# Performance work log

Measured on AMD Instinct MI355X. Metric: run time of the kernel, lower is better.

## Reference

```python
import jax, jax.numpy as jnp
import numpy as np

N, CH, K, B = 30000, 96, 81, 8
HIDDEN = max(CH // 4, 8)
EPS = 1e-5


def setup_inputs() -> dict:
    key = jax.random.key(0)
    ks = jax.random.split(key, 12)
    feats = jax.random.normal(ks[0], (N, CH), dtype=jnp.float32)
    nbr_idx = jax.random.randint(ks[1], (N, K), 0, N).astype(jnp.int32)
    batch_ids = jnp.sort(jax.random.randint(ks[2], (N,), 0, B)).astype(jnp.int32)
    s = 1.0 / np.sqrt(CH * 1.0)
    W1 = jax.random.normal(ks[3], (K, CH, CH), dtype=jnp.float32) * s
    W2 = jax.random.normal(ks[4], (K, CH, CH), dtype=jnp.float32) * s
    g1 = jnp.ones((CH,), jnp.float32); b1 = jnp.zeros((CH,), jnp.float32)
    g2 = jnp.ones((CH,), jnp.float32); b2 = jnp.zeros((CH,), jnp.float32)
    fc1_w = jax.random.normal(ks[5], (CH, HIDDEN), dtype=jnp.float32) * s
    fc1_b = jnp.zeros((HIDDEN,), jnp.float32)
    fc2_w = jax.random.normal(ks[6], (HIDDEN, CH), dtype=jnp.float32) * (1.0 / np.sqrt(HIDDEN * 1.0))
    fc2_b = jnp.zeros((CH,), jnp.float32)
    return {"feats": feats, "W1": W1, "g1": g1, "b1": b1, "W2": W2,
            "g2": g2, "b2": b2, "fc1_w": fc1_w, "fc1_b": fc1_b,
            "fc2_w": fc2_w, "fc2_b": fc2_b, "nbr_idx": nbr_idx,
            "batch_ids": batch_ids}


def _sparse_conv(x, W, nbr):
    # gather-matmul-scatter form of MinkowskiConvolution (kernel map shared):
    # g: [N, K, ch] gathered neighbor features; contract each offset's [ch,ch] weight.
    g = x[nbr]
    return jnp.einsum('nkc,kcd->nd', g, W)


def _bn(x, gamma, beta):
    mu = jnp.mean(x, axis=0)
    var = jnp.var(x, axis=0)
    return gamma * (x - mu) * jax.lax.rsqrt(var + EPS) + beta


def _se(x, batch_ids, fc1_w, fc1_b, fc2_w, fc2_b):
    # MinkowskiGlobalAvgPooling: per-sample mean over points
    sums = jax.ops.segment_sum(x, batch_ids, num_segments=B)
    cnts = jax.ops.segment_sum(jnp.ones((x.shape[0], 1), x.dtype), batch_ids, num_segments=B)
    pooled = sums / jnp.maximum(cnts, 1.0)  # [B, ch]
    w = jax.nn.relu(pooled @ fc1_w + fc1_b)
    w = jax.nn.sigmoid(w @ fc2_w + fc2_b)   # [B, ch]
    return x * w[batch_ids]                  # broadcast multiplication


def reference(feats, W1, g1, b1, W2, g2, b2, fc1_w, fc1_b, fc2_w, fc2_b,
              nbr_idx, batch_ids):
    out = jax.nn.relu(_bn(_sparse_conv(feats, W1, nbr_idx), g1, b1))
    out = _bn(_sparse_conv(out, W2, nbr_idx), g2, b2)
    out = _se(out, batch_ids, fc1_w, fc1_b, fc2_w, fc2_b)
    return jax.nn.relu(out + feats)
```

## Files before the change

### kernel.cpp

```cpp
#include <hip/hip_runtime.h>
#include <hip/hip_bf16.h>

#define NPTS 30000
#define CH 96
#define KOFF 81
#define NB 8
#define HID 24
#define EPSV 1e-5f
#define NTILE 469
#define KSPLIT 3
#define KPER 27

typedef __attribute__((ext_vector_type(8))) short bf16x8;
typedef __attribute__((ext_vector_type(4))) float f32x4;

__device__ __forceinline__ ushort f2bf(float f) {
    union { float f; unsigned int u; } x; x.f = f;
    unsigned int u = x.u;
    unsigned int r = (u + 0x7fffu + ((u >> 16) & 1u)) >> 16;
    return (ushort)r;
}

__device__ __forceinline__ void gll16(const void* g, void* l) {
    __builtin_amdgcn_global_load_lds(
        (const __attribute__((address_space(1))) unsigned int*)g,
        (__attribute__((address_space(3))) unsigned int*)l, 16, 0, 0);
}


__global__ void k_cvt_feats(const float* __restrict__ in, ushort* __restrict__ out, int n4) {
    int t = blockIdx.x * 256 + threadIdx.x;
    if (t >= n4) return;
    float4 v = reinterpret_cast<const float4*>(in)[t];
    ushort4 o;
    o.x = f2bf(v.x); o.y = f2bf(v.y); o.z = f2bf(v.z); o.w = f2bf(v.w);
    reinterpret_cast<ushort4*>(out)[t] = o;
}

__global__ void k_cvt_w(const float* __restrict__ W1, const float* __restrict__ W2,
                        ushort* __restrict__ wt1, ushort* __restrict__ wt2) {
    __shared__ float lds[9216];
    int b = blockIdx.x;
    int k = (b < 81) ? b : b - 81;
    const float* src = ((b < 81) ? W1 : W2) + k * 9216;
    ushort* dst = ((b < 81) ? wt1 : wt2) + k * 9216;
    for (int j = threadIdx.x; j < 9216; j += 256) lds[j] = src[j];
    __syncthreads();
    for (int o = threadIdx.x; o < 9216; o += 256) {
        int q = o / 768, rem = o - q * 768, d = rem >> 3, j = rem & 7;
        dst[o] = f2bf(lds[(q * 8 + j) * 96 + d]);
    }
}

__global__ void k_nbrT(const int* __restrict__ nbr, int* __restrict__ nbrT) {
    __shared__ int lds[64 * 81];
    int n0 = blockIdx.x * 64;
    int rows = min(64, NPTS - n0);
    int cnt = rows * 81;
    for (int i = threadIdx.x; i < cnt; i += 256) lds[i] = nbr[n0 * 81 + i];
    __syncthreads();
    for (int o = threadIdx.x; o < cnt; o += 256) {
        int kk = o / rows, r = o - kk * rows;
        nbrT[kk * NPTS + n0 + r] = lds[r * 81 + kk];
    }
}

__global__ void k_cnt(const int* __restrict__ bids, float* __restrict__ cnt) {
    __shared__ int h[NB];
    if (threadIdx.x < NB) h[threadIdx.x] = 0;
    __syncthreads();
    int n = blockIdx.x * 256 + threadIdx.x;
    if (n < NPTS) atomicAdd(&h[bids[n]], 1);
    __syncthreads();
    if (threadIdx.x < NB && h[threadIdx.x]) atomicAdd(&cnt[threadIdx.x], (float)h[threadIdx.x]);
}

__global__ __launch_bounds__(256, 5) void k_conv(const ushort* __restrict__ xbf,
                                                 const ushort* __restrict__ wt,
                                                 const int* __restrict__ nbrT,
                                                 float* __restrict__ out) {
    __shared__ __align__(16) ushort Asm[12 * 64 * 8];
    __shared__ __align__(16) ushort Wsm[12 * 96 * 8];

    const int tid = threadIdx.x;
    const int tile = blockIdx.x % NTILE;
    const int slice = blockIdx.x / NTILE;
    const int n0 = tile * 64;
    const int wave = tid >> 6, lane = tid & 63;
    const int r16 = lane & 15, kg = lane >> 4;
    const int k0 = slice * KPER, k1 = k0 + KPER;

    f32x4 zero4 = {0.f, 0.f, 0.f, 0.f};
    f32x4 acc[6];
#pragma unroll
    for (int i = 0; i < 6; ++i) acc[i] = zero4;

    const int nrow = n0 + lane;
    const bool rowok = (nrow < NPTS);
    int idxnext = rowok ? nbrT[k0 * NPTS + nrow] : 0;

    for (int k = k0; k < k1; ++k) {
        int idx = idxnext;
        if (k + 1 < k1) idxnext = rowok ? nbrT[(k + 1) * NPTS + nrow] : 0;

        const ushort* asrc = xbf + idx * 96;
#pragma unroll
        for (int t = 0; t < 3; ++t) {
            int q = wave + t * 4;
            gll16(asrc + q * 8, Asm + q * 512);
        }
        const ushort* wsrc = wt + k * 9216 + lane * 8;
#pragma unroll
        for (int t = 0; t < 5; ++t) {
            int i = wave + t * 4;
            if (i < 18) gll16(wsrc + i * 512, Wsm + i * 512);
        }
        __syncthreads();

#pragma unroll
        for (int c = 0; c < 3; ++c) {
            int q = c * 4 + kg;
            bf16x8 a = *reinterpret_cast<const bf16x8*>(Asm + q * 512 + (wave * 16 + r16) * 8);
#pragma unroll
            for (int db = 0; db < 6; ++db) {
                bf16x8 b = *reinterpret_cast<const bf16x8*>(Wsm + q * 768 + (db * 16 + r16) * 8);
                acc[db] = __builtin_amdgcn_mfma_f32_16x16x32_bf16(a, b, acc[db], 0, 0, 0);
            }
        }
        __syncthreads();
    }

#pragma unroll
    for (int db = 0; db < 6; ++db) {
        int col = db * 16 + r16;
#pragma unroll
        for (int i = 0; i < 4; ++i) {
            int r = wave * 16 + kg * 4 + i;
            if (n0 + r < NPTS) atomicAdd(&out[(n0 + r) * 96 + col], acc[db][i]);
        }
    }
}

__global__ __launch_bounds__(256) void k_stats(const float* __restrict__ y,
                                               float* __restrict__ ssum, float* __restrict__ ssq) {
    __shared__ float ls[96], lq[96];
    int tid = threadIdx.x;
    if (tid < 96) { ls[tid] = 0.f; lq[tid] = 0.f; }
    __syncthreads();
    for (int i = blockIdx.x * 256 + tid; i < NPTS * CH / 4; i += 256 * 256) {
        float4 v = reinterpret_cast<const float4*>(y)[i];
        int d0 = (i * 4) % 96;
        atomicAdd(&ls[d0], v.x);     atomicAdd(&lq[d0], v.x * v.x);
        atomicAdd(&ls[d0 + 1], v.y); atomicAdd(&lq[d0 + 1], v.y * v.y);
        atomicAdd(&ls[d0 + 2], v.z); atomicAdd(&lq[d0 + 2], v.z * v.z);
        atomicAdd(&ls[d0 + 3], v.w); atomicAdd(&lq[d0 + 3], v.w * v.w);
    }
    __syncthreads();
    if (tid < 96) { atomicAdd(&ssum[tid], ls[tid]); atomicAdd(&ssq[tid], lq[tid]); }
}

__global__ void k_bnfinal(const float* __restrict__ ssum, const float* __restrict__ ssq,
                          const float* __restrict__ g, const float* __restrict__ b,
                          float* __restrict__ scale, float* __restrict__ shift) {
    int t = threadIdx.x;
    if (t >= 96) return;
    float mean = ssum[t] * (1.0f / NPTS);
    float var = ssq[t] * (1.0f / NPTS) - mean * mean;
    float sc = g[t] * rsqrtf(var + EPSV);
    scale[t] = sc;
    shift[t] = b[t] - mean * sc;
}

__global__ void k_apply1(const float* __restrict__ x, const float* __restrict__ scale,
                         const float* __restrict__ shift, ushort* __restrict__ h, int n4) {
    int t = blockIdx.x * 256 + threadIdx.x;
    if (t >= n4) return;
    float4 v = reinterpret_cast<const float4*>(x)[t];
    int d0 = (t * 4) % 96;
    ushort4 o;
    o.x = f2bf(fmaxf(v.x * scale[d0] + shift[d0], 0.f));
    o.y = f2bf(fmaxf(v.y * scale[d0 + 1] + shift[d0 + 1], 0.f));
    o.z = f2bf(fmaxf(v.z * scale[d0 + 2] + shift[d0 + 2], 0.f));
    o.w = f2bf(fmaxf(v.w * scale[d0 + 3] + shift[d0 + 3], 0.f));
    reinterpret_cast<ushort4*>(h)[t] = o;
}

__global__ void k_segsum(const float* __restrict__ out2, const float* __restrict__ scale,
                         const float* __restrict__ shift, const int* __restrict__ bids,
                         float* __restrict__ segsum) {
    int d = threadIdx.x;
    if (d >= 96) return;
    int n0 = blockIdx.x * 64;
    int rows = min(64, NPTS - n0);
    float sc = scale[d], sh = shift[d];
    int cur = bids[n0];
    float acc = 0.f;
    for (int r = 0; r < rows; ++r) {
        int n = n0 + r;
        int b = bids[n];
        if (b != cur) { atomicAdd(&segsum[cur * 96 + d], acc); acc = 0.f; cur = b; }
        acc += out2[n * 96 + d] * sc + sh;
    }
    atomicAdd(&segsum[cur * 96 + d], acc);
}

__global__ void k_se(const float* __restrict__ segsum, const float* __restrict__ cnt,
                     const float* __restrict__ fc1w, const float* __restrict__ fc1b,
                     const float* __restrict__ fc2w, const float* __restrict__ fc2b,
                     float* __restrict__ sew) {
    __shared__ float pooled[NB][96];
    __shared__ float hid[NB][HID];
    int t = threadIdx.x;
    for (int i = t; i < NB * 96; i += 256) {
        int b = i / 96, d = i - b * 96;
        pooled[b][d] = segsum[i] / fmaxf(cnt[b], 1.f);
    }
    __syncthreads();
    if (t < NB * HID) {
        int b = t / HID, h = t - b * HID;
        float s = fc1b[h];
        for (int d = 0; d < 96; ++d) s += pooled[b][d] * fc1w[d * HID + h];
        hid[b][h] = fmaxf(s, 0.f);
    }
    __syncthreads();
    for (int i = t; i < NB * 96; i += 256) {
        int b = i / 96, d = i - b * 96;
        float s = fc2b[d];
        for (int h = 0; h < HID; ++h) s += hid[b][h] * fc2w[h * 96 + d];
        sew[i] = 1.f / (1.f + expf(-s));
    }
}

__global__ void k_final(const float* __restrict__ out2, const float* __restrict__ feats,
                        const float* __restrict__ scale, const float* __restrict__ shift,
                        const float* __restrict__ sew, const int* __restrict__ bids,
                        float* __restrict__ out, int n4) {
    int t = blockIdx.x * 256 + threadIdx.x;
    if (t >= n4) return;
    int e0 = t * 4;
    int n = e0 / 96;
    int d0 = e0 - n * 96;
    int b = bids[n];
    const float* w = sew + b * 96;
    float4 v = reinterpret_cast<const float4*>(out2)[t];
    float4 f = reinterpret_cast<const float4*>(feats)[t];
    float4 o;
    o.x = fmaxf((v.x * scale[d0] + shift[d0]) * w[d0] + f.x, 0.f);
    o.y = fmaxf((v.y * scale[d0 + 1] + shift[d0 + 1]) * w[d0 + 1] + f.y, 0.f);
    o.z = fmaxf((v.z * scale[d0 + 2] + shift[d0 + 2]) * w[d0 + 2] + f.z, 0.f);
    o.w = fmaxf((v.w * scale[d0 + 3] + shift[d0 + 3]) * w[d0 + 3] + f.w, 0.f);
    reinterpret_cast<float4*>(out)[t] = o;
}


extern "C" void kernel_launch(void* const* d_in, const int* in_sizes, int n_in,
                              void* d_out, int out_size, void* d_ws, size_t ws_size,
                              hipStream_t stream) {
    const float* feats = (const float*)d_in[0];
    const float* W1 = (const float*)d_in[1];
    const float* g1 = (const float*)d_in[2];
    const float* b1 = (const float*)d_in[3];
    const float* W2 = (const float*)d_in[4];
    const float* g2 = (const float*)d_in[5];
    const float* b2 = (const float*)d_in[6];
    const float* fc1w = (const float*)d_in[7];
    const float* fc1b = (const float*)d_in[8];
    const float* fc2w = (const float*)d_in[9];
    const float* fc2b = (const float*)d_in[10];
    const int* nbr = (const int*)d_in[11];
    const int* bids = (const int*)d_in[12];
    float* out = (float*)d_out;

    char* ws = (char*)d_ws;
    ushort* featsbf = (ushort*)(ws + 0);
    ushort* wt1 = (ushort*)(ws + 5760000);
    ushort* wt2 = (ushort*)(ws + 7252992);
    int* nbrT = (int*)(ws + 8745984);
    float* outbuf = (float*)(ws + 18465984);
    ushort* h1bf = (ushort*)(ws + 29985984);
    float* small = (float*)(ws + 35745984);
    float* sum1 = small + 0;
    float* sq1 = small + 96;
    float* sum2 = small + 192;
    float* sq2 = small + 288;
    float* scale1 = small + 384;
    float* shift1 = small + 480;
    float* scale2 = small + 576;
    float* shift2 = small + 672;
    float* segsum = small + 768;
    float* cntf = small + 1536;
    float* sew = small + 1544;

    const int n4 = NPTS * CH / 4;
    const int gE = (n4 + 255) / 256;
    const int gC = NTILE * KSPLIT;

    hipMemsetAsync(small, 0, 16384, stream);
    hipMemsetAsync(outbuf, 0, NPTS * CH * 4, stream);
    k_cvt_feats<<<gE, 256, 0, stream>>>(feats, featsbf, n4);
    k_cvt_w<<<162, 256, 0, stream>>>(W1, W2, wt1, wt2);
    k_nbrT<<<NTILE, 256, 0, stream>>>(nbr, nbrT);
    k_cnt<<<(NPTS + 255) / 256, 256, 0, stream>>>(bids, cntf);

    k_conv<<<gC, 256, 0, stream>>>(featsbf, wt1, nbrT, outbuf);
    k_stats<<<256, 256, 0, stream>>>(outbuf, sum1, sq1);
    k_bnfinal<<<1, 128, 0, stream>>>(sum1, sq1, g1, b1, scale1, shift1);
    k_apply1<<<gE, 256, 0, stream>>>(outbuf, scale1, shift1, h1bf, n4);

    hipMemsetAsync(outbuf, 0, NPTS * CH * 4, stream);
    k_conv<<<gC, 256, 0, stream>>>(h1bf, wt2, nbrT, outbuf);
    k_stats<<<256, 256, 0, stream>>>(outbuf, sum2, sq2);
    k_bnfinal<<<1, 128, 0, stream>>>(sum2, sq2, g2, b2, scale2, shift2);

    k_segsum<<<NTILE, 128, 0, stream>>>(outbuf, scale2, shift2, bids, segsum);
    k_se<<<1, 256, 0, stream>>>(segsum, cntf, fc1w, fc1b, fc2w, fc2b, sew);
    k_final<<<gE, 256, 0, stream>>>(outbuf, feats, scale2, shift2, sew, bids, out, n4);
}
```

Before: 426.3 us.

## Restructure sparse conv tiling, fuse prep kernels, and fold segment-sum into stats

The conv kernel now has each block handle three 64-row tiles over a 20-21 offset slice. Weight tiles are double-buffered in LDS and reused across the row tiles, and neighbor features are loaded straight from global memory into registers instead of through LDS. The feature/weight/index conversion kernels and the output zeroing are merged into one prep launch, and the second zeroing moves into the apply kernel. The second stats pass computes per-batch segment sums by binary-searching the sorted batch ids, which removes the separate segsum and count kernels. The aim is fewer launches, less weight reloading per block and less synchronisation, at the cost of lower occupancy (launch bounds 2) and uncoalesced direct gathers.

```diff
diff --git a/kernel.cpp b/kernel.cpp
--- a/kernel.cpp
+++ b/kernel.cpp
@@ -8,8 +8,9 @@
 #define HID 24
 #define EPSV 1e-5f
 #define NTILE 469
-#define KSPLIT 3
-#define KPER 27
+#define RT 3
+#define RSPLIT 157
+#define KSPLIT 4
 
 typedef __attribute__((ext_vector_type(8))) short bf16x8;
 typedef __attribute__((ext_vector_type(4))) float f32x4;
@@ -27,136 +28,210 @@
         (__attribute__((address_space(3))) unsigned int*)l, 16, 0, 0);
 }
 
-
-__global__ void k_cvt_feats(const float* __restrict__ in, ushort* __restrict__ out, int n4) {
-    int t = blockIdx.x * 256 + threadIdx.x;
-    if (t >= n4) return;
-    float4 v = reinterpret_cast<const float4*>(in)[t];
-    ushort4 o;
-    o.x = f2bf(v.x); o.y = f2bf(v.y); o.z = f2bf(v.z); o.w = f2bf(v.w);
-    reinterpret_cast<ushort4*>(out)[t] = o;
-}
-
-__global__ void k_cvt_w(const float* __restrict__ W1, const float* __restrict__ W2,
-                        ushort* __restrict__ wt1, ushort* __restrict__ wt2) {
-    __shared__ float lds[9216];
-    int b = blockIdx.x;
-    int k = (b < 81) ? b : b - 81;
-    const float* src = ((b < 81) ? W1 : W2) + k * 9216;
-    ushort* dst = ((b < 81) ? wt1 : wt2) + k * 9216;
-    for (int j = threadIdx.x; j < 9216; j += 256) lds[j] = src[j];
-    __syncthreads();
-    for (int o = threadIdx.x; o < 9216; o += 256) {
-        int q = o / 768, rem = o - q * 768, d = rem >> 3, j = rem & 7;
-        dst[o] = f2bf(lds[(q * 8 + j) * 96 + d]);
-    }
-}
-
-__global__ void k_nbrT(const int* __restrict__ nbr, int* __restrict__ nbrT) {
-    __shared__ int lds[64 * 81];
-    int n0 = blockIdx.x * 64;
-    int rows = min(64, NPTS - n0);
-    int cnt = rows * 81;
-    for (int i = threadIdx.x; i < cnt; i += 256) lds[i] = nbr[n0 * 81 + i];
-    __syncthreads();
-    for (int o = threadIdx.x; o < cnt; o += 256) {
-        int kk = o / rows, r = o - kk * rows;
-        nbrT[kk * NPTS + n0 + r] = lds[r * 81 + kk];
-    }
-}
-
-__global__ void k_cnt(const int* __restrict__ bids, float* __restrict__ cnt) {
-    __shared__ int h[NB];
-    if (threadIdx.x < NB) h[threadIdx.x] = 0;
-    __syncthreads();
-    int n = blockIdx.x * 256 + threadIdx.x;
-    if (n < NPTS) atomicAdd(&h[bids[n]], 1);
-    __syncthreads();
-    if (threadIdx.x < NB && h[threadIdx.x]) atomicAdd(&cnt[threadIdx.x], (float)h[threadIdx.x]);
-}
-
-__global__ __launch_bounds__(256, 5) void k_conv(const ushort* __restrict__ xbf,
+__global__ __launch_bounds__(256) void k_prep(const float* __restrict__ feats,
+                                              const float* __restrict__ W1,
+                                              const float* __restrict__ W2,
+                                              const int* __restrict__ nbr,
+                                              ushort* __restrict__ featsbf,
+                                              float* __restrict__ outbuf,
+                                              int* __restrict__ nbrT,
+                                              ushort* __restrict__ wt1,
+                                              ushort* __restrict__ wt2) {
+    __shared__ __align__(16) char smem[36864];
+    int bid = blockIdx.x, tid = threadIdx.x;
+    if (bid < 2813) {
+        int t = bid * 256 + tid;
+        if (t < 720000) {
+            float4 v = reinterpret_cast<const float4*>(feats)[t];
+            ushort4 o;
+            o.x = f2bf(v.x); o.y = f2bf(v.y); o.z = f2bf(v.z); o.w = f2bf(v.w);
+            reinterpret_cast<ushort4*>(featsbf)[t] = o;
+            float4 z = {0.f, 0.f, 0.f, 0.f};
+            reinterpret_cast<float4*>(outbuf)[t] = z;
+        }
+    } else if (bid < 3282) {
+        int* lds = (int*)smem;
+        int n0 = (bid - 2813) * 64;
+        int rows = min(64, NPTS - n0);
+        int cnt = rows * 81;
+        for (int i = tid; i < cnt; i += 256) lds[i] = nbr[n0 * 81 + i];
+        __syncthreads();
+        for (int o = tid; o < cnt; o += 256) {
+            int kk = o / rows, r = o - kk * rows;
+            nbrT[kk * NPTS + n0 + r] = lds[r * 81 + kk];
+        }
+    } else {
+        float* lds = (float*)smem;
+        int b = bid - 3282;
+        int k = (b < 81) ? b : b - 81;
+        const float* src = ((b < 81) ? W1 : W2) + k * 9216;
+        ushort* dst = ((b < 81) ? wt1 : wt2) + k * 9216;
+        for (int j = tid; j < 9216; j += 256) lds[j] = src[j];
+        __syncthreads();
+        for (int o = tid; o < 9216; o += 256) {
+            int q = o / 768, rem = o - q * 768, d = rem >> 3, j = rem & 7;
+            dst[o] = f2bf(lds[(q * 8 + j) * 96 + d]);
+        }
+    }
+}
+
+__global__ __launch_bounds__(256, 2) void k_conv(const ushort* __restrict__ xbf,
                                                  const ushort* __restrict__ wt,
                                                  const int* __restrict__ nbrT,
                                                  float* __restrict__ out) {
-    __shared__ __align__(16) ushort Asm[12 * 64 * 8];
-    __shared__ __align__(16) ushort Wsm[12 * 96 * 8];
+    __shared__ __align__(16) ushort Wsm[2][9216];
 
     const int tid = threadIdx.x;
-    const int tile = blockIdx.x % NTILE;
-    const int slice = blockIdx.x / NTILE;
-    const int n0 = tile * 64;
+    const int slice = blockIdx.x / RSPLIT;
+    const int rb = blockIdx.x % RSPLIT;
+    const int k0 = slice * 20;
+    const int k1 = k0 + ((slice == 3) ? 21 : 20);
     const int wave = tid >> 6, lane = tid & 63;
     const int r16 = lane & 15, kg = lane >> 4;
-    const int k0 = slice * KPER, k1 = k0 + KPER;
+    const int tile0 = rb * RT;
+
+    int nrow[RT];
+#pragma unroll
+    for (int rt = 0; rt < RT; ++rt) {
+        int n = (tile0 + rt) * 64 + wave * 16 + r16;
+        nrow[rt] = (n < NPTS) ? n : (NPTS - 1);
+    }
 
     f32x4 zero4 = {0.f, 0.f, 0.f, 0.f};
-    f32x4 acc[6];
-#pragma unroll
-    for (int i = 0; i < 6; ++i) acc[i] = zero4;
-
-    const int nrow = n0 + lane;
-    const bool rowok = (nrow < NPTS);
-    int idxnext = rowok ? nbrT[k0 * NPTS + nrow] : 0;
-
-    for (int k = k0; k < k1; ++k) {
-        int idx = idxnext;
-        if (k + 1 < k1) idxnext = rowok ? nbrT[(k + 1) * NPTS + nrow] : 0;
-
-        const ushort* asrc = xbf + idx * 96;
-#pragma unroll
-        for (int t = 0; t < 3; ++t) {
-            int q = wave + t * 4;
-            gll16(asrc + q * 8, Asm + q * 512);
-        }
-        const ushort* wsrc = wt + k * 9216 + lane * 8;
+    f32x4 acc[RT][6];
+#pragma unroll
+    for (int rt = 0; rt < RT; ++rt)
+#pragma unroll
+        for (int db = 0; db < 6; ++db) acc[rt][db] = zero4;
+
+    {
+        const ushort* wsrc = wt + k0 * 9216 + lane * 8;
 #pragma unroll
         for (int t = 0; t < 5; ++t) {
             int i = wave + t * 4;
-            if (i < 18) gll16(wsrc + i * 512, Wsm + i * 512);
-        }
-        __syncthreads();
-
+            if (i < 18) gll16(wsrc + i * 512, Wsm[0] + i * 512);
+        }
+    }
+    int idx[RT];
+#pragma unroll
+    for (int rt = 0; rt < RT; ++rt) idx[rt] = nbrT[k0 * NPTS + nrow[rt]];
+    __syncthreads();
+
+    int cur = 0;
+    for (int k = k0; k < k1; ++k) {
+        bf16x8 bfrag[18];
 #pragma unroll
         for (int c = 0; c < 3; ++c) {
             int q = c * 4 + kg;
-            bf16x8 a = *reinterpret_cast<const bf16x8*>(Asm + q * 512 + (wave * 16 + r16) * 8);
-#pragma unroll
-            for (int db = 0; db < 6; ++db) {
-                bf16x8 b = *reinterpret_cast<const bf16x8*>(Wsm + q * 768 + (db * 16 + r16) * 8);
-                acc[db] = __builtin_amdgcn_mfma_f32_16x16x32_bf16(a, b, acc[db], 0, 0, 0);
+#pragma unroll
+            for (int db = 0; db < 6; ++db)
+                bfrag[c * 6 + db] = *reinterpret_cast<const bf16x8*>(
+                    &Wsm[cur][q * 768 + (db * 16 + r16) * 8]);
+        }
+        bf16x8 afrag[RT][3];
+#pragma unroll
+        for (int rt = 0; rt < RT; ++rt) {
+            const ushort* as = xbf + idx[rt] * 96 + kg * 8;
+#pragma unroll
+            for (int c = 0; c < 3; ++c)
+                afrag[rt][c] = *reinterpret_cast<const bf16x8*>(as + c * 32);
+        }
+        if (k + 1 < k1) {
+            const ushort* wsrc = wt + (k + 1) * 9216 + lane * 8;
+#pragma unroll
+            for (int t = 0; t < 5; ++t) {
+                int i = wave + t * 4;
+                if (i < 18) gll16(wsrc + i * 512, Wsm[cur ^ 1] + i * 512);
             }
-        }
+#pragma unroll
+            for (int rt = 0; rt < RT; ++rt) idx[rt] = nbrT[(k + 1) * NPTS + nrow[rt]];
+        }
+#pragma unroll
+        for (int rt = 0; rt < RT; ++rt)
+#pragma unroll
+            for (int c = 0; c < 3; ++c)
+#pragma unroll
+                for (int db = 0; db < 6; ++db)
+                    acc[rt][db] = __builtin_amdgcn_mfma_f32_16x16x32_bf16(
+                        afrag[rt][c], bfrag[c * 6 + db], acc[rt][db], 0, 0, 0);
         __syncthreads();
-    }
-
-#pragma unroll
-    for (int db = 0; db < 6; ++db) {
-        int col = db * 16 + r16;
-#pragma unroll
-        for (int i = 0; i < 4; ++i) {
-            int r = wave * 16 + kg * 4 + i;
-            if (n0 + r < NPTS) atomicAdd(&out[(n0 + r) * 96 + col], acc[db][i]);
-        }
-    }
-}
-
+        cur ^= 1;
+    }
+
+#pragma unroll
+    for (int rt = 0; rt < RT; ++rt) {
+        int rbase = (tile0 + rt) * 64 + wave * 16 + kg * 4;
+#pragma unroll
+        for (int db = 0; db < 6; ++db) {
+            int col = db * 16 + r16;
+#pragma unroll
+            for (int i = 0; i < 4; ++i) {
+                int r = rbase + i;
+                if (r < NPTS) atomicAdd(&out[r * 96 + col], acc[rt][db][i]);
+            }
+        }
+    }
+}
+
+__device__ __forceinline__ int lowb(const int* __restrict__ bids, int v) {
+    int lo = 0, hi = NPTS;
+    while (lo < hi) { int m = (lo + hi) >> 1; if (bids[m] < v) lo = m + 1; else hi = m; }
+    return lo;
+}
+
+template <bool SEG>
 __global__ __launch_bounds__(256) void k_stats(const float* __restrict__ y,
-                                               float* __restrict__ ssum, float* __restrict__ ssq) {
-    __shared__ float ls[96], lq[96];
+                                               const int* __restrict__ bids,
+                                               float* __restrict__ ssum,
+                                               float* __restrict__ ssq,
+                                               float* __restrict__ segsum,
+                                               float* __restrict__ cntf) {
+    __shared__ float ls[96], lq[96], lg[96];
     int tid = threadIdx.x;
-    if (tid < 96) { ls[tid] = 0.f; lq[tid] = 0.f; }
-    __syncthreads();
-    for (int i = blockIdx.x * 256 + tid; i < NPTS * CH / 4; i += 256 * 256) {
-        float4 v = reinterpret_cast<const float4*>(y)[i];
-        int d0 = (i * 4) % 96;
-        atomicAdd(&ls[d0], v.x);     atomicAdd(&lq[d0], v.x * v.x);
-        atomicAdd(&ls[d0 + 1], v.y); atomicAdd(&lq[d0 + 1], v.y * v.y);
-        atomicAdd(&ls[d0 + 2], v.z); atomicAdd(&lq[d0 + 2], v.z * v.z);
-        atomicAdd(&ls[d0 + 3], v.w); atomicAdd(&lq[d0 + 3], v.w * v.w);
-    }
-    __syncthreads();
-    if (tid < 96) { atomicAdd(&ssum[tid], ls[tid]); atomicAdd(&ssq[tid], lq[tid]); }
+    if (tid < 96) { ls[tid] = 0.f; lq[tid] = 0.f; lg[tid] = 0.f; }
+    __syncthreads();
+
+    int b = 0, j, s, e;
+    if (SEG) {
+        b = blockIdx.x >> 5; j = blockIdx.x & 31;
+        s = lowb(bids, b); e = lowb(bids, b + 1);
+    } else {
+        j = blockIdx.x; s = 0; e = NPTS;
+    }
+    const int stride = SEG ? (32 * 256) : (256 * 256);
+    const int total = (e - s) * 24;
+    const int base4 = s * 24;
+    const int c40 = j * 256 + tid;
+
+    f32x4 z = {0.f, 0.f, 0.f, 0.f};
+    f32x4 sm[3] = {z, z, z}, sq[3] = {z, z, z};
+    for (int c4 = c40; c4 < total; c4 += 3 * stride) {
+#pragma unroll
+        for (int m = 0; m < 3; ++m) {
+            int c = c4 + m * stride;
+            if (c < total) {
+                f32x4 v = reinterpret_cast<const f32x4*>(y)[base4 + c];
+                sm[m] += v; sq[m] += v * v;
+            }
+        }
+    }
+#pragma unroll
+    for (int m = 0; m < 3; ++m) {
+        int d0 = ((c40 + m * stride) * 4) % 96;
+#pragma unroll
+        for (int w = 0; w < 4; ++w) {
+            atomicAdd(&ls[d0 + w], sm[m][w]);
+            atomicAdd(&lq[d0 + w], sq[m][w]);
+            if (SEG) atomicAdd(&lg[d0 + w], sm[m][w]);
+        }
+    }
+    __syncthreads();
+    if (tid < 96) {
+        atomicAdd(&ssum[tid], ls[tid]);
+        atomicAdd(&ssq[tid], lq[tid]);
+        if (SEG) atomicAdd(&segsum[b * 96 + tid], lg[tid]);
+    }
+    if (SEG && tid == 0 && (blockIdx.x & 31) == 0) cntf[b] = (float)(e - s);
 }
 
 __global__ void k_bnfinal(const float* __restrict__ ssum, const float* __restrict__ ssq,
@@ -171,10 +246,10 @@
     shift[t] = b[t] - mean * sc;
 }
 
-__global__ void k_apply1(const float* __restrict__ x, const float* __restrict__ scale,
-                         const float* __restrict__ shift, ushort* __restrict__ h, int n4) {
+__global__ void k_apply1(float* __restrict__ x, const float* __restrict__ scale,
+                         const float* __restrict__ shift, ushort* __restrict__ h) {
     int t = blockIdx.x * 256 + threadIdx.x;
-    if (t >= n4) return;
+    if (t >= 720000) return;
     float4 v = reinterpret_cast<const float4*>(x)[t];
     int d0 = (t * 4) % 96;
     ushort4 o;
@@ -183,28 +258,12 @@
     o.z = f2bf(fmaxf(v.z * scale[d0 + 2] + shift[d0 + 2], 0.f));
     o.w = f2bf(fmaxf(v.w * scale[d0 + 3] + shift[d0 + 3], 0.f));
     reinterpret_cast<ushort4*>(h)[t] = o;
-}
-
-__global__ void k_segsum(const float* __restrict__ out2, const float* __restrict__ scale,
-                         const float* __restrict__ shift, const int* __restrict__ bids,
-                         float* __restrict__ segsum) {
-    int d = threadIdx.x;
-    if (d >= 96) return;
-    int n0 = blockIdx.x * 64;
-    int rows = min(64, NPTS - n0);
-    float sc = scale[d], sh = shift[d];
-    int cur = bids[n0];
-    float acc = 0.f;
-    for (int r = 0; r < rows; ++r) {
-        int n = n0 + r;
-        int b = bids[n];
-        if (b != cur) { atomicAdd(&segsum[cur * 96 + d], acc); acc = 0.f; cur = b; }
-        acc += out2[n * 96 + d] * sc + sh;
-    }
-    atomicAdd(&segsum[cur * 96 + d], acc);
+    float4 z = {0.f, 0.f, 0.f, 0.f};
+    reinterpret_cast<float4*>(x)[t] = z;
 }
 
 __global__ void k_se(const float* __restrict__ segsum, const float* __restrict__ cnt,
+                     const float* __restrict__ scale, const float* __restrict__ shift,
                      const float* __restrict__ fc1w, const float* __restrict__ fc1b,
                      const float* __restrict__ fc2w, const float* __restrict__ fc2b,
                      float* __restrict__ sew) {
@@ -213,7 +272,7 @@
     int t = threadIdx.x;
     for (int i = t; i < NB * 96; i += 256) {
         int b = i / 96, d = i - b * 96;
-        pooled[b][d] = segsum[i] / fmaxf(cnt[b], 1.f);
+        pooled[b][d] = segsum[i] / fmaxf(cnt[b], 1.f) * scale[d] + shift[d];
     }
     __syncthreads();
     if (t < NB * HID) {
@@ -234,9 +293,9 @@
 __global__ void k_final(const float* __restrict__ out2, const float* __restrict__ feats,
                         const float* __restrict__ scale, const float* __restrict__ shift,
                         const float* __restrict__ sew, const int* __restrict__ bids,
-                        float* __restrict__ out, int n4) {
+                        float* __restrict__ out) {
     int t = blockIdx.x * 256 + threadIdx.x;
-    if (t >= n4) return;
+    if (t >= 720000) return;
     int e0 = t * 4;
     int n = e0 / 96;
     int d0 = e0 - n * 96;
@@ -291,28 +350,21 @@
     float* cntf = small + 1536;
     float* sew = small + 1544;
 
-    const int n4 = NPTS * CH / 4;
-    const int gE = (n4 + 255) / 256;
-    const int gC = NTILE * KSPLIT;
+    const int gE = 2813;
+    const int gC = KSPLIT * RSPLIT;
 
     hipMemsetAsync(small, 0, 16384, stream);
-    hipMemsetAsync(outbuf, 0, NPTS * CH * 4, stream);
-    k_cvt_feats<<<gE, 256, 0, stream>>>(feats, featsbf, n4);
-    k_cvt_w<<<162, 256, 0, stream>>>(W1, W2, wt1, wt2);
-    k_nbrT<<<NTILE, 256, 0, stream>>>(nbr, nbrT);
-    k_cnt<<<(NPTS + 255) / 256, 256, 0, stream>>>(bids, cntf);
+    k_prep<<<3444, 256, 0, stream>>>(feats, W1, W2, nbr, featsbf, outbuf, nbrT, wt1, wt2);
 
     k_conv<<<gC, 256, 0, stream>>>(featsbf, wt1, nbrT, outbuf);
-    k_stats<<<256, 256, 0, stream>>>(outbuf, sum1, sq1);
+    k_stats<false><<<256, 256, 0, stream>>>(outbuf, bids, sum1, sq1, segsum, cntf);
     k_bnfinal<<<1, 128, 0, stream>>>(sum1, sq1, g1, b1, scale1, shift1);
-    k_apply1<<<gE, 256, 0, stream>>>(outbuf, scale1, shift1, h1bf, n4);
-
-    hipMemsetAsync(outbuf, 0, NPTS * CH * 4, stream);
+    k_apply1<<<gE, 256, 0, stream>>>(outbuf, scale1, shift1, h1bf);
+
     k_conv<<<gC, 256, 0, stream>>>(h1bf, wt2, nbrT, outbuf);
-    k_stats<<<256, 256, 0, stream>>>(outbuf, sum2, sq2);
+    k_stats<true><<<256, 256, 0, stream>>>(outbuf, bids, sum2, sq2, segsum, cntf);
     k_bnfinal<<<1, 128, 0, stream>>>(sum2, sq2, g2, b2, scale2, shift2);
 
-    k_segsum<<<NTILE, 128, 0, stream>>>(outbuf, scale2, shift2, bids, segsum);
-    k_se<<<1, 256, 0, stream>>>(segsum, cntf, fc1w, fc1b, fc2w, fc2b, sew);
-    k_final<<<gE, 256, 0, stream>>>(outbuf, feats, scale2, shift2, sew, bids, out, n4);
-}
+    k_se<<<1, 256, 0, stream>>>(segsum, cntf, scale2, shift2, fc1w, fc1b, fc2w, fc2b, sew);
+    k_final<<<gE, 256, 0, stream>>>(outbuf, feats, scale2, shift2, sew, bids, out);
+}
```

Result: faster. 370.8 us (-13.0%).
